# Optimization experiments

Measured on AMD Instinct MI355X. Metric: run time of the kernel, lower is better.

## Reference

```python
import jax, jax.numpy as jnp
import numpy as np

N_NODES = 50000


def _sage_conv(x, edge_index, Wl, bl, Wr):
    # PyG SAGEConv with mean aggregation:
    #   out_i = Wl @ mean_{j in N(i)} x_j + bl + Wr @ x_i
    src, dst = edge_index[0], edge_index[1]
    msgs = x[src]                                            # [E, d] gather
    summed = jax.ops.segment_sum(msgs, dst, num_segments=N_NODES)   # [N, d]
    count = jax.ops.segment_sum(jnp.ones((edge_index.shape[1],), x.dtype),
                                dst, num_segments=N_NODES)          # [N]
    agg = summed / jnp.maximum(count, 1.0)[:, None]          # mean, 0 for isolated nodes
    return agg @ Wl.T + bl + x @ Wr.T


def setup_inputs() -> dict:
    key = jax.random.key(0)
    k1, k2, k3, k4, k5 = jax.random.split(key, 5)
    d = 128
    E = 640000
    x = jax.random.normal(k1, (N_NODES, d), dtype=jnp.float32)
    edge_index = jax.random.randint(k2, (2, E), 0, N_NODES, dtype=jnp.int64)
    s = 1.0 / np.sqrt(d)
    Wl = jax.random.uniform(k3, (d, d), jnp.float32, -s, s)
    bl = jax.random.uniform(k4, (d,), jnp.float32, -s, s)
    Wr = jax.random.uniform(k5, (d, d), jnp.float32, -s, s)
    return {"x": x, "edge_index": edge_index, "Wl": Wl, "bl": bl, "Wr": Wr}


def reference(x, edge_index, Wl, bl, Wr):
    # forward in the source applies conv1 twice (conv2 is unused)
    h = _sage_conv(x, edge_index, Wl, bl, Wr)
    h = jax.nn.relu(h)
    h = _sage_conv(h, edge_index, Wl, bl, Wr)
    return h
```

## Files before the change

kernel.cpp:

```cpp
#include <hip/hip_runtime.h>

#define NN 50000
#define D 128

typedef short bf16x8 __attribute__((ext_vector_type(8)));
typedef float f32x16 __attribute__((ext_vector_type(16)));

__device__ __forceinline__ unsigned bf16r(float f) {
    unsigned u = __float_as_uint(f);
    return (u + 0x7FFFu + ((u >> 16) & 1u)) >> 16;
}
__device__ __forceinline__ float bflo(unsigned u) { return __uint_as_float(u << 16); }
__device__ __forceinline__ float bfhi(unsigned u) { return __uint_as_float(u & 0xFFFF0000u); }


__global__ void zero_k(uint4* __restrict__ p, int nq) {
    int i = blockIdx.x * 256 + threadIdx.x;
    if (i < nq) { uint4 z = {0, 0, 0, 0}; p[i] = z; }
}


__global__ void hist_k(const int* __restrict__ ei, int E, int* __restrict__ count) {
    int e = blockIdx.x * 256 + threadIdx.x;
    if (e < E) atomicAdd(&count[ei[E + e]], 1);
}

__global__ void chunk_sum_k(const int* __restrict__ count, int n, int* __restrict__ partial) {
    int i = blockIdx.x * 256 + threadIdx.x;
    int v = (i < n) ? count[i] : 0;
    for (int off = 32; off; off >>= 1) v += __shfl_down(v, off);
    __shared__ int ws[4];
    int lane = threadIdx.x & 63, wave = threadIdx.x >> 6;
    if (lane == 0) ws[wave] = v;
    __syncthreads();
    if (threadIdx.x == 0) partial[blockIdx.x] = ws[0] + ws[1] + ws[2] + ws[3];
}

__global__ void scan_block_k(int* partial, int nchunk) {
    __shared__ int sm[256];
    int t = threadIdx.x;
    int v = (t < nchunk) ? partial[t] : 0;
    sm[t] = v;
    __syncthreads();
    for (int off = 1; off < 256; off <<= 1) {
        int add = (t >= off) ? sm[t - off] : 0;
        __syncthreads();
        sm[t] += add;
        __syncthreads();
    }
    if (t < nchunk) partial[t] = sm[t] - v;
}

__global__ void rowptr_k(const int* __restrict__ count, const int* __restrict__ partial,
                         int n, int* __restrict__ rowptr) {
    int i = blockIdx.x * 256 + threadIdx.x;
    int c = (i < n) ? count[i] : 0;
    int lane = threadIdx.x & 63, wave = threadIdx.x >> 6;
    int incl = c;
    for (int off = 1; off < 64; off <<= 1) {
        int nv = __shfl_up(incl, off);
        if (lane >= off) incl += nv;
    }
    __shared__ int ws[4];
    if (lane == 63) ws[wave] = incl;
    __syncthreads();
    int base = 0;
    for (int w = 0; w < 3; ++w) if (w < wave) base += ws[w];
    if (i < n) rowptr[i] = partial[blockIdx.x] + base + incl - c;
}

__global__ void fill_k(const int* __restrict__ ei, int E,
                       const int* __restrict__ rowptr, int* __restrict__ count,
                       int* __restrict__ csr) {
    int e = blockIdx.x * 256 + threadIdx.x;
    if (e < E) {
        int d = ei[E + e];
        int slot = atomicSub(&count[d], 1) - 1;
        csr[rowptr[d] + slot] = ei[e];
    }
}


__global__ void wtb_k(const float* __restrict__ Wl, const float* __restrict__ Wr,
                      uint* __restrict__ wb) {
    int i = blockIdx.x * 256 + threadIdx.x;
    if (i >= 128 * 128) return;
    int nrow = i >> 7;
    int k = (i & 127) * 2;
    const float* W = (k < 128) ? Wl : Wr;
    int kk = k & 127;
    uint lo = bf16r(W[nrow * 128 + kk]);
    uint hi = bf16r(W[nrow * 128 + kk + 1]);
    wb[i] = (hi << 16) | lo;
}


__global__ void cvt_k(const float* __restrict__ in, uint* __restrict__ out, int nquad) {
    int i = blockIdx.x * 256 + threadIdx.x;
    if (i >= nquad) return;
    float4 v = ((const float4*)in)[i];
    uint2 p;
    p.x = (bf16r(v.y) << 16) | bf16r(v.x);
    p.y = (bf16r(v.w) << 16) | bf16r(v.z);
    ((uint2*)out)[i] = p;
}


__global__ __launch_bounds__(256) void fused_layer_k(
    const uint4* __restrict__ in4,
    const int* __restrict__ rowptr,
    const int* __restrict__ csr,
    const ushort* __restrict__ Wb,
    const float* __restrict__ bl,
    float* __restrict__ out,
    ushort* __restrict__ hb,
    int N, int E, int relu) {
    __shared__ uint4 At[32][16];

    int tid = threadIdx.x;
    int mt  = blockIdx.x;

    int lnode = tid >> 4;
    int c16   = tid & 15;
    #pragma unroll
    for (int g = 0; g < 2; ++g) {
        int lrow = g * 16 + lnode;
        int n = mt * 32 + lrow;
        float s0=0,s1=0,s2=0,s3=0,s4=0,s5=0,s6=0,s7=0;
        float inv = 0.f;
        if (n < N) {
            int ro = rowptr[n];
            int re = (n == N - 1) ? E : rowptr[n + 1];
            int deg = re - ro;
            int i = 0;
            for (; i + 4 <= deg; i += 4) {
                int e0 = csr[ro + i],     e1 = csr[ro + i + 1];
                int e2 = csr[ro + i + 2], e3 = csr[ro + i + 3];
                uint4 v0 = in4[(size_t)e0 * 16 + c16];
                uint4 v1 = in4[(size_t)e1 * 16 + c16];
                uint4 v2 = in4[(size_t)e2 * 16 + c16];
                uint4 v3 = in4[(size_t)e3 * 16 + c16];
                s0 += bflo(v0.x)+bflo(v1.x)+bflo(v2.x)+bflo(v3.x);
                s1 += bfhi(v0.x)+bfhi(v1.x)+bfhi(v2.x)+bfhi(v3.x);
                s2 += bflo(v0.y)+bflo(v1.y)+bflo(v2.y)+bflo(v3.y);
                s3 += bfhi(v0.y)+bfhi(v1.y)+bfhi(v2.y)+bfhi(v3.y);
                s4 += bflo(v0.z)+bflo(v1.z)+bflo(v2.z)+bflo(v3.z);
                s5 += bfhi(v0.z)+bfhi(v1.z)+bfhi(v2.z)+bfhi(v3.z);
                s6 += bflo(v0.w)+bflo(v1.w)+bflo(v2.w)+bflo(v3.w);
                s7 += bfhi(v0.w)+bfhi(v1.w)+bfhi(v2.w)+bfhi(v3.w);
            }
            for (; i < deg; ++i) {
                uint4 v0 = in4[(size_t)csr[ro + i] * 16 + c16];
                s0 += bflo(v0.x); s1 += bfhi(v0.x);
                s2 += bflo(v0.y); s3 += bfhi(v0.y);
                s4 += bflo(v0.z); s5 += bfhi(v0.z);
                s6 += bflo(v0.w); s7 += bfhi(v0.w);
            }
            inv = (deg > 0) ? (1.f / (float)deg) : 0.f;
        }
        uint4 r;
        r.x = (bf16r(s1 * inv) << 16) | bf16r(s0 * inv);
        r.y = (bf16r(s3 * inv) << 16) | bf16r(s2 * inv);
        r.z = (bf16r(s5 * inv) << 16) | bf16r(s4 * inv);
        r.w = (bf16r(s7 * inv) << 16) | bf16r(s6 * inv);
        At[lrow][c16 ^ (lrow & 7)] = r;
    }
    __syncthreads();

    int wid   = tid >> 6;
    int lane  = tid & 63;
    int col   = lane & 31;
    int khalf = lane >> 5;
    int nfeat = wid * 32 + col;

    bf16x8 B[16], A[16];
    const ushort* wrow = Wb + (size_t)nfeat * 256 + khalf * 8;
    #pragma unroll
    for (int ks = 0; ks < 16; ++ks)
        B[ks] = *reinterpret_cast<const bf16x8*>(wrow + ks * 16);

    #pragma unroll
    for (int ks = 0; ks < 8; ++ks) {
        int cc = (ks * 2 + khalf) ^ (col & 7);
        A[ks] = *reinterpret_cast<const bf16x8*>(&At[col][cc]);
    }
    int rowc = min(mt * 32 + col, N - 1);
    const ushort* ar1 = (const ushort*)in4 + (size_t)rowc * 128 + khalf * 8;
    #pragma unroll
    for (int ks = 0; ks < 8; ++ks)
        A[8 + ks] = *reinterpret_cast<const bf16x8*>(ar1 + ks * 16);

    f32x16 acc = {};
    #pragma unroll
    for (int ks = 0; ks < 16; ++ks)
        acc = __builtin_amdgcn_mfma_f32_32x32x16_bf16(A[ks], B[ks], acc, 0, 0, 0);

    float bias = bl[nfeat];
    #pragma unroll
    for (int r = 0; r < 16; ++r) {
        int rr = (r & 3) + 8 * (r >> 2) + 4 * khalf;
        int gm = mt * 32 + rr;
        if (gm < N) {
            float v = acc[r] + bias;
            if (relu) v = fmaxf(v, 0.f);
            if (out) out[(size_t)gm * 128 + nfeat] = v;
            if (hb)  hb[(size_t)gm * 128 + nfeat] = (ushort)bf16r(v);
        }
    }
}

extern "C" void kernel_launch(void* const* d_in, const int* in_sizes, int n_in,
                              void* d_out, int out_size, void* d_ws, size_t ws_size,
                              hipStream_t stream) {
    const float* x  = (const float*)d_in[0];
    const int*   ei = (const int*)d_in[1];
    const float* Wl = (const float*)d_in[2];
    const float* bl = (const float*)d_in[3];
    const float* Wr = (const float*)d_in[4];
    float* out = (float*)d_out;

    const int N = NN;
    const int E = in_sizes[1] / 2;
    const int NPAD = 50016;

    int* ws      = (int*)d_ws;
    int* count   = ws;
    int* rowptr  = ws + N;
    int* partial = ws + 2 * N;
    int* csr     = ws + 2 * N + 256;
    uint* wb     = (uint*)(ws + 2 * N + 256 + E);
    uint* xb     = wb + 128 * 128;
    uint* hb     = xb + (size_t)NPAD * 64;

    int eb = (E + 255) / 256;
    int nchunk = (N + 255) / 256;

    zero_k<<<(N / 4 + 255) / 256, 256, 0, stream>>>((uint4*)count, N / 4);
    hist_k<<<eb, 256, 0, stream>>>(ei, E, count);
    chunk_sum_k<<<nchunk, 256, 0, stream>>>(count, N, partial);
    scan_block_k<<<1, 256, 0, stream>>>(partial, nchunk);
    rowptr_k<<<nchunk, 256, 0, stream>>>(count, partial, N, rowptr);
    fill_k<<<eb, 256, 0, stream>>>(ei, E, rowptr, count, csr);
    wtb_k<<<64, 256, 0, stream>>>(Wl, Wr, wb);
    cvt_k<<<(N * 32 + 255) / 256, 256, 0, stream>>>(x, xb, N * 32);

    int mtiles = (N + 31) / 32;
    fused_layer_k<<<mtiles, 256, 0, stream>>>((const uint4*)xb, rowptr, csr,
                                              (const ushort*)wb, bl,
                                              (float*)nullptr, (ushort*)hb, N, E, 1);
    fused_layer_k<<<mtiles, 256, 0, stream>>>((const uint4*)hb, rowptr, csr,
                                              (const ushort*)wb, bl,
                                              out, (ushort*)nullptr, N, E, 0);
}
```

Measured before the change: 171.2 us.

## Sort nodes by degree for load-balanced tiles, widen aggregation to 512 threads

Builds a degree histogram and counting-sort permutation so each 32-node tile holds nodes of similar in-degree, which reduces wave divergence in the gather loop. The fused layer kernel now uses 512 threads, one thread group per node instead of two sequential passes, and unrolls the gather loop 8-wide for more memory parallelism. Outputs are scattered back through the permutation. It also merges the weight and input conversion kernels into one launch. This adds a scatter kernel, atomics for bucket offsets, and non-contiguous output writes and root-feature reads.

```diff
diff --git a/kernel.cpp b/kernel.cpp
--- a/kernel.cpp
+++ b/kernel.cpp
@@ -25,30 +25,46 @@
     if (e < E) atomicAdd(&count[ei[E + e]], 1);
 }
 
-__global__ void chunk_sum_k(const int* __restrict__ count, int n, int* __restrict__ partial) {
-    int i = blockIdx.x * 256 + threadIdx.x;
-    int v = (i < n) ? count[i] : 0;
-    for (int off = 32; off; off >>= 1) v += __shfl_down(v, off);
+__global__ void chunk_sum_k(const int* __restrict__ count, int n,
+                            int* __restrict__ partial, int* __restrict__ dhist) {
+    __shared__ int dh[256];
+    int t = threadIdx.x;
+    dh[t] = 0;
+    __syncthreads();
+    int i = blockIdx.x * 256 + t;
+    int v = 0;
+    if (i < n) {
+        v = count[i];
+        atomicAdd(&dh[min(v, 255)], 1);
+    }
+    int s = v;
+    for (int off = 32; off; off >>= 1) s += __shfl_down(s, off);
     __shared__ int ws[4];
-    int lane = threadIdx.x & 63, wave = threadIdx.x >> 6;
-    if (lane == 0) ws[wave] = v;
-    __syncthreads();
-    if (threadIdx.x == 0) partial[blockIdx.x] = ws[0] + ws[1] + ws[2] + ws[3];
-}
-
-__global__ void scan_block_k(int* partial, int nchunk) {
+    int lane = t & 63, wave = t >> 6;
+    if (lane == 0) ws[wave] = s;
+    __syncthreads();
+    if (t == 0) partial[blockIdx.x] = ws[0] + ws[1] + ws[2] + ws[3];
+    if (dh[t]) atomicAdd(&dhist[t], dh[t]);
+}
+
+__global__ void scan_block_k(int* partial, int nchunk,
+                             const int* __restrict__ dhist, int* __restrict__ bucketOff) {
     __shared__ int sm[256];
+    __shared__ int sm2[256];
     int t = threadIdx.x;
     int v = (t < nchunk) ? partial[t] : 0;
-    sm[t] = v;
+    int r = dhist[255 - t];
+    sm[t] = v; sm2[t] = r;
     __syncthreads();
     for (int off = 1; off < 256; off <<= 1) {
-        int add = (t >= off) ? sm[t - off] : 0;
+        int a = (t >= off) ? sm[t - off] : 0;
+        int b = (t >= off) ? sm2[t - off] : 0;
         __syncthreads();
-        sm[t] += add;
+        sm[t] += a; sm2[t] += b;
         __syncthreads();
     }
     if (t < nchunk) partial[t] = sm[t] - v;
+    bucketOff[255 - t] = sm2[t] - r;
 }
 
 __global__ void rowptr_k(const int* __restrict__ count, const int* __restrict__ partial,
@@ -69,6 +85,16 @@
     if (i < n) rowptr[i] = partial[blockIdx.x] + base + incl - c;
 }
 
+__global__ void scatter_k(const int* __restrict__ count, int* __restrict__ bucketOff,
+                          int* __restrict__ perm, int N) {
+    int i = blockIdx.x * 256 + threadIdx.x;
+    if (i < N) {
+        int d = min(count[i], 255);
+        int pos = atomicAdd(&bucketOff[d], 1);
+        perm[pos] = i;
+    }
+}
+
 __global__ void fill_k(const int* __restrict__ ei, int E,
                        const int* __restrict__ rowptr, int* __restrict__ count,
                        int* __restrict__ csr) {
@@ -81,35 +107,39 @@
 }
 
 
-__global__ void wtb_k(const float* __restrict__ Wl, const float* __restrict__ Wr,
-                      uint* __restrict__ wb) {
-    int i = blockIdx.x * 256 + threadIdx.x;
-    if (i >= 128 * 128) return;
-    int nrow = i >> 7;
-    int k = (i & 127) * 2;
-    const float* W = (k < 128) ? Wl : Wr;
-    int kk = k & 127;
-    uint lo = bf16r(W[nrow * 128 + kk]);
-    uint hi = bf16r(W[nrow * 128 + kk + 1]);
-    wb[i] = (hi << 16) | lo;
-}
-
-
-__global__ void cvt_k(const float* __restrict__ in, uint* __restrict__ out, int nquad) {
-    int i = blockIdx.x * 256 + threadIdx.x;
-    if (i >= nquad) return;
-    float4 v = ((const float4*)in)[i];
-    uint2 p;
-    p.x = (bf16r(v.y) << 16) | bf16r(v.x);
-    p.y = (bf16r(v.w) << 16) | bf16r(v.z);
-    ((uint2*)out)[i] = p;
-}
-
-
-__global__ __launch_bounds__(256) void fused_layer_k(
+__global__ void wtbcvt_k(const float* __restrict__ Wl, const float* __restrict__ Wr,
+                         uint* __restrict__ wb,
+                         const float* __restrict__ x, uint* __restrict__ xb, int nquad) {
+    if (blockIdx.x < 64) {
+        int i = blockIdx.x * 256 + threadIdx.x;
+        int nrow = i >> 7;
+        int k = (i & 127) * 2;
+        const float* W = (k < 128) ? Wl : Wr;
+        int kk = k & 127;
+        uint lo = bf16r(W[nrow * 128 + kk]);
+        uint hi = bf16r(W[nrow * 128 + kk + 1]);
+        wb[i] = (hi << 16) | lo;
+    } else {
+        int i = (blockIdx.x - 64) * 256 + threadIdx.x;
+        if (i >= nquad) return;
+        float4 v = ((const float4*)x)[i];
+        uint2 p;
+        p.x = (bf16r(v.y) << 16) | bf16r(v.x);
+        p.y = (bf16r(v.w) << 16) | bf16r(v.z);
+        ((uint2*)xb)[i] = p;
+    }
+}
+
+
+#define ACC8(v)                                                         \
+    s0 += bflo(v.x); s1 += bfhi(v.x); s2 += bflo(v.y); s3 += bfhi(v.y); \
+    s4 += bflo(v.z); s5 += bfhi(v.z); s6 += bflo(v.w); s7 += bfhi(v.w);
+
+__global__ __launch_bounds__(512, 8) void fused_layer_k(
     const uint4* __restrict__ in4,
     const int* __restrict__ rowptr,
     const int* __restrict__ csr,
+    const int* __restrict__ perm,
     const ushort* __restrict__ Wb,
     const float* __restrict__ bl,
     float* __restrict__ out,
@@ -120,52 +150,52 @@
     int tid = threadIdx.x;
     int mt  = blockIdx.x;
 
-    int lnode = tid >> 4;
-    int c16   = tid & 15;
-    #pragma unroll
-    for (int g = 0; g < 2; ++g) {
-        int lrow = g * 16 + lnode;
-        int n = mt * 32 + lrow;
-        float s0=0,s1=0,s2=0,s3=0,s4=0,s5=0,s6=0,s7=0;
-        float inv = 0.f;
-        if (n < N) {
-            int ro = rowptr[n];
-            int re = (n == N - 1) ? E : rowptr[n + 1];
-            int deg = re - ro;
-            int i = 0;
-            for (; i + 4 <= deg; i += 4) {
-                int e0 = csr[ro + i],     e1 = csr[ro + i + 1];
-                int e2 = csr[ro + i + 2], e3 = csr[ro + i + 3];
-                uint4 v0 = in4[(size_t)e0 * 16 + c16];
-                uint4 v1 = in4[(size_t)e1 * 16 + c16];
-                uint4 v2 = in4[(size_t)e2 * 16 + c16];
-                uint4 v3 = in4[(size_t)e3 * 16 + c16];
-                s0 += bflo(v0.x)+bflo(v1.x)+bflo(v2.x)+bflo(v3.x);
-                s1 += bfhi(v0.x)+bfhi(v1.x)+bfhi(v2.x)+bfhi(v3.x);
-                s2 += bflo(v0.y)+bflo(v1.y)+bflo(v2.y)+bflo(v3.y);
-                s3 += bfhi(v0.y)+bfhi(v1.y)+bfhi(v2.y)+bfhi(v3.y);
-                s4 += bflo(v0.z)+bflo(v1.z)+bflo(v2.z)+bflo(v3.z);
-                s5 += bfhi(v0.z)+bfhi(v1.z)+bfhi(v2.z)+bfhi(v3.z);
-                s6 += bflo(v0.w)+bflo(v1.w)+bflo(v2.w)+bflo(v3.w);
-                s7 += bfhi(v0.w)+bfhi(v1.w)+bfhi(v2.w)+bfhi(v3.w);
-            }
-            for (; i < deg; ++i) {
-                uint4 v0 = in4[(size_t)csr[ro + i] * 16 + c16];
-                s0 += bflo(v0.x); s1 += bfhi(v0.x);
-                s2 += bflo(v0.y); s3 += bfhi(v0.y);
-                s4 += bflo(v0.z); s5 += bfhi(v0.z);
-                s6 += bflo(v0.w); s7 += bfhi(v0.w);
-            }
-            inv = (deg > 0) ? (1.f / (float)deg) : 0.f;
-        }
-        uint4 r;
-        r.x = (bf16r(s1 * inv) << 16) | bf16r(s0 * inv);
-        r.y = (bf16r(s3 * inv) << 16) | bf16r(s2 * inv);
-        r.z = (bf16r(s5 * inv) << 16) | bf16r(s4 * inv);
-        r.w = (bf16r(s7 * inv) << 16) | bf16r(s6 * inv);
-        At[lrow][c16 ^ (lrow & 7)] = r;
-    }
-    __syncthreads();
+    int lrow = tid >> 4;
+    int c16  = tid & 15;
+    int n    = mt * 32 + lrow;
+    float s0=0,s1=0,s2=0,s3=0,s4=0,s5=0,s6=0,s7=0;
+    float inv = 0.f;
+    if (n < N) {
+        int prow = perm[n];
+        int ro = rowptr[prow];
+        int re = (prow == N - 1) ? E : rowptr[prow + 1];
+        int deg = re - ro;
+        int i = 0;
+        for (; i + 8 <= deg; i += 8) {
+            int e0 = csr[ro+i+0], e1 = csr[ro+i+1], e2 = csr[ro+i+2], e3 = csr[ro+i+3];
+            int e4 = csr[ro+i+4], e5 = csr[ro+i+5], e6 = csr[ro+i+6], e7 = csr[ro+i+7];
+            uint4 v0 = in4[(size_t)e0 * 16 + c16];
+            uint4 v1 = in4[(size_t)e1 * 16 + c16];
+            uint4 v2 = in4[(size_t)e2 * 16 + c16];
+            uint4 v3 = in4[(size_t)e3 * 16 + c16];
+            uint4 v4 = in4[(size_t)e4 * 16 + c16];
+            uint4 v5 = in4[(size_t)e5 * 16 + c16];
+            uint4 v6 = in4[(size_t)e6 * 16 + c16];
+            uint4 v7 = in4[(size_t)e7 * 16 + c16];
+            ACC8(v0); ACC8(v1); ACC8(v2); ACC8(v3);
+            ACC8(v4); ACC8(v5); ACC8(v6); ACC8(v7);
+        }
+        for (; i + 2 <= deg; i += 2) {
+            int e0 = csr[ro + i], e1 = csr[ro + i + 1];
+            uint4 v0 = in4[(size_t)e0 * 16 + c16];
+            uint4 v1 = in4[(size_t)e1 * 16 + c16];
+            ACC8(v0); ACC8(v1);
+        }
+        if (i < deg) {
+            uint4 v0 = in4[(size_t)csr[ro + i] * 16 + c16];
+            ACC8(v0);
+        }
+        inv = (deg > 0) ? (1.f / (float)deg) : 0.f;
+    }
+    uint4 r;
+    r.x = (bf16r(s1 * inv) << 16) | bf16r(s0 * inv);
+    r.y = (bf16r(s3 * inv) << 16) | bf16r(s2 * inv);
+    r.z = (bf16r(s5 * inv) << 16) | bf16r(s4 * inv);
+    r.w = (bf16r(s7 * inv) << 16) | bf16r(s6 * inv);
+    At[lrow][c16 ^ (lrow & 7)] = r;
+    __syncthreads();
+
+    if (tid >= 256) return;
 
     int wid   = tid >> 6;
     int lane  = tid & 63;
@@ -184,7 +214,8 @@
         int cc = (ks * 2 + khalf) ^ (col & 7);
         A[ks] = *reinterpret_cast<const bf16x8*>(&At[col][cc]);
     }
-    int rowc = min(mt * 32 + col, N - 1);
+    int aidx = mt * 32 + col;
+    int rowc = (aidx < N) ? perm[aidx] : 0;
     const ushort* ar1 = (const ushort*)in4 + (size_t)rowc * 128 + khalf * 8;
     #pragma unroll
     for (int ks = 0; ks < 8; ++ks)
@@ -197,14 +228,15 @@
 
     float bias = bl[nfeat];
     #pragma unroll
-    for (int r = 0; r < 16; ++r) {
-        int rr = (r & 3) + 8 * (r >> 2) + 4 * khalf;
-        int gm = mt * 32 + rr;
-        if (gm < N) {
-            float v = acc[r] + bias;
+    for (int r2 = 0; r2 < 16; ++r2) {
+        int rr = (r2 & 3) + 8 * (r2 >> 2) + 4 * khalf;
+        int idx = mt * 32 + rr;
+        if (idx < N) {
+            int gp = perm[idx];
+            float v = acc[r2] + bias;
             if (relu) v = fmaxf(v, 0.f);
-            if (out) out[(size_t)gm * 128 + nfeat] = v;
-            if (hb)  hb[(size_t)gm * 128 + nfeat] = (ushort)bf16r(v);
+            if (out) out[(size_t)gp * 128 + nfeat] = v;
+            if (hb)  hb[(size_t)gp * 128 + nfeat] = (ushort)bf16r(v);
         }
     }
 }
@@ -223,32 +255,35 @@
     const int E = in_sizes[1] / 2;
     const int NPAD = 50016;
 
-    int* ws      = (int*)d_ws;
-    int* count   = ws;
-    int* rowptr  = ws + N;
-    int* partial = ws + 2 * N;
-    int* csr     = ws + 2 * N + 256;
-    uint* wb     = (uint*)(ws + 2 * N + 256 + E);
-    uint* xb     = wb + 128 * 128;
-    uint* hb     = xb + (size_t)NPAD * 64;
+    int* ws        = (int*)d_ws;
+    int* count     = ws;
+    int* dhist     = ws + N;
+    int* bucketOff = ws + N + 256;
+    int* rowptr    = ws + N + 512;
+    int* partial   = ws + 2 * N + 512;
+    int* perm      = ws + 2 * N + 768;
+    int* csr       = perm + NPAD;
+    uint* wb       = (uint*)(csr + E);
+    uint* xb       = wb + 128 * 128;
+    uint* hb       = xb + (size_t)NPAD * 64;
 
     int eb = (E + 255) / 256;
     int nchunk = (N + 255) / 256;
 
-    zero_k<<<(N / 4 + 255) / 256, 256, 0, stream>>>((uint4*)count, N / 4);
+    zero_k<<<((N + 256) / 4 + 255) / 256, 256, 0, stream>>>((uint4*)count, (N + 256) / 4);
     hist_k<<<eb, 256, 0, stream>>>(ei, E, count);
-    chunk_sum_k<<<nchunk, 256, 0, stream>>>(count, N, partial);
-    scan_block_k<<<1, 256, 0, stream>>>(partial, nchunk);
+    chunk_sum_k<<<nchunk, 256, 0, stream>>>(count, N, partial, dhist);
+    scan_block_k<<<1, 256, 0, stream>>>(partial, nchunk, dhist, bucketOff);
     rowptr_k<<<nchunk, 256, 0, stream>>>(count, partial, N, rowptr);
+    scatter_k<<<nchunk, 256, 0, stream>>>(count, bucketOff, perm, N);
     fill_k<<<eb, 256, 0, stream>>>(ei, E, rowptr, count, csr);
-    wtb_k<<<64, 256, 0, stream>>>(Wl, Wr, wb);
-    cvt_k<<<(N * 32 + 255) / 256, 256, 0, stream>>>(x, xb, N * 32);
+    wtbcvt_k<<<64 + (N * 32 + 255) / 256, 256, 0, stream>>>(Wl, Wr, wb, x, xb, N * 32);
 
     int mtiles = (N + 31) / 32;
-    fused_layer_k<<<mtiles, 256, 0, stream>>>((const uint4*)xb, rowptr, csr,
+    fused_layer_k<<<mtiles, 512, 0, stream>>>((const uint4*)xb, rowptr, csr, perm,
                                               (const ushort*)wb, bl,
                                               (float*)nullptr, (ushort*)hb, N, E, 1);
-    fused_layer_k<<<mtiles, 256, 0, stream>>>((const uint4*)hb, rowptr, csr,
+    fused_layer_k<<<mtiles, 512, 0, stream>>>((const uint4*)hb, rowptr, csr, perm,
                                               (const ushort*)wb, bl,
                                               out, (ushort*)nullptr, N, E, 0);
 }
```

Result: slower. 400.7 us (+134.0%).
